# Kernel optimization log

Measured on AMD Instinct MI355X. Metric: run time of the kernel, lower is better.

## Reference

```python
import jax, jax.numpy as jnp
import numpy as np

N_LABELS = 16
LABEL_DIM = 128
BN_EPS = 1e-5


def setup_inputs() -> dict:
    key = jax.random.key(0)
    k1, k2 = jax.random.split(key, 2)
    B, T, D = 8, 512, 768
    return {
        "features": jax.random.normal(k1, (B, T, D), dtype=jnp.float32),
        "mask": jnp.ones((B, T), dtype=bool),
        "bn_gamma": jnp.ones((D,), dtype=jnp.float32),
        "bn_beta": jnp.zeros((D,), dtype=jnp.float32),
        "ff_w": jax.random.normal(k2, (LABEL_DIM * N_LABELS * 2, D), dtype=jnp.float32) * 0.02,
        "ff_b": jnp.zeros((LABEL_DIM * N_LABELS * 2,), dtype=jnp.float32),
        "label_bias": jnp.zeros((N_LABELS,), dtype=jnp.float32),
    }


def reference(features, mask, bn_gamma, bn_beta, ff_w, ff_b, label_bias):
    B, T, D = features.shape
    m = mask.astype(features.dtype)[..., None]  # [B,T,1]
    denom = jnp.maximum(m.sum(), 1.0)
    # FlatBatchNorm (training mode): stats over masked tokens, zeros elsewhere
    mean = (features * m).sum(axis=(0, 1)) / denom
    var = (((features - mean) ** 2) * m).sum(axis=(0, 1)) / denom
    normed = (features - mean) * jax.lax.rsqrt(var + BN_EPS) * bn_gamma + bn_beta
    feats = normed * m  # res[mask]=flat, zeros elsewhere
    # FFN + relu -> [B,T,n_labels,label_dim,2]
    h = jax.nn.relu(jnp.einsum('btd,od->bto', feats, ff_w) + ff_b)
    h = h.reshape(B, T, N_LABELS, LABEL_DIM, 2)
    start_f = h[..., 0]  # [B,T,L,D]
    end_f = h[..., 1]
    # biaffine span scores: [B, L, T_start, T_end]
    scores = jnp.einsum('bsld,beld->blse', start_f, end_f) + label_bias[None, :, None, None]
    triu = jnp.triu(jnp.ones((T, T), dtype=bool))
    spans_mask = triu[None, None] & mask[:, None, :, None] & mask[:, None, None, :]  # [B,L,T,T] via broadcast
    spans_mask = jnp.broadcast_to(spans_mask, scores.shape)
    return scores, spans_mask
```

## Files before the change

kernel.cpp:

```cpp
#include <hip/hip_runtime.h>

#define B_    8
#define T_    512
#define D_    768
#define L_    16
#define DL_   128
#define NO_   4096
#define M_    4096
#define BN_EPS 1e-5f

typedef __attribute__((ext_vector_type(8))) short short8;
typedef __attribute__((ext_vector_type(4))) float f32x4;

__device__ inline unsigned short f2bf(float x) {
    unsigned int u = __float_as_uint(x);
    unsigned int r = (u + 0x7fffu + ((u >> 16) & 1u)) >> 16;
    return (unsigned short)r;
}

__device__ __forceinline__ void gload_lds16(const unsigned short* g, unsigned short* l) {
    __builtin_amdgcn_global_load_lds(
        (const __attribute__((address_space(1))) unsigned int*)g,
        (__attribute__((address_space(3))) unsigned int*)l, 16, 0, 0);
}

__global__ void k_stats(const float* __restrict__ f, const int* __restrict__ mask,
                        float* __restrict__ stats) {
    int tid = threadIdx.x;
    int t0  = blockIdx.x * 16;
    float s0 = 0.f, s1 = 0.f, s2 = 0.f, q0 = 0.f, q1 = 0.f, q2 = 0.f;
    for (int tt = 0; tt < 16; ++tt) {
        int t = t0 + tt;
        float m = mask[t] ? 1.f : 0.f;
        const float* row = f + (size_t)t * D_;
        float x0 = row[tid];
        float x1 = row[tid + 256];
        float x2 = row[tid + 512];
        s0 += x0 * m; q0 += x0 * x0 * m;
        s1 += x1 * m; q1 += x1 * x1 * m;
        s2 += x2 * m; q2 += x2 * x2 * m;
    }
    atomicAdd(&stats[tid      ], s0);
    atomicAdd(&stats[tid + 256], s1);
    atomicAdd(&stats[tid + 512], s2);
    atomicAdd(&stats[768 + tid      ], q0);
    atomicAdd(&stats[768 + tid + 256], q1);
    atomicAdd(&stats[768 + tid + 512], q2);
    if (tid == 0) {
        int c = 0;
        for (int tt = 0; tt < 16; ++tt) c += (mask[t0 + tt] ? 1 : 0);
        atomicAdd(&stats[1536], (float)c);
    }
}

__global__ void k_finalize(const float* __restrict__ gamma, const float* __restrict__ beta,
                           float* __restrict__ stats) {
    int d = threadIdx.x;
    float denom = fmaxf(stats[1536], 1.f);
    float mean  = stats[d] / denom;
    float var   = fmaxf(stats[768 + d] / denom - mean * mean, 0.f);
    float sc    = gamma[d] * rsqrtf(var + BN_EPS);
    stats[2048 + d] = sc;
    stats[2816 + d] = beta[d] - mean * sc;
}

__global__ void k_normcast(const float4* __restrict__ f4, const float4* __restrict__ w4,
                           const int* __restrict__ mask, const float* __restrict__ stats,
                           unsigned short* __restrict__ featp, unsigned short* __restrict__ wp) {
    int i = blockIdx.x * 256 + threadIdx.x;
    if (i < M_ * D_ / 4) {
        int d4 = i % (D_ / 4);
        int t  = i / (D_ / 4);
        float m = mask[t] ? 1.f : 0.f;
        float4 v = f4[i];
        int d = d4 * 4;
        float r0 = (v.x * stats[2048 + d + 0] + stats[2816 + d + 0]) * m;
        float r1 = (v.y * stats[2048 + d + 1] + stats[2816 + d + 1]) * m;
        float r2 = (v.z * stats[2048 + d + 2] + stats[2816 + d + 2]) * m;
        float r3 = (v.w * stats[2048 + d + 3] + stats[2816 + d + 3]) * m;
        ushort4 o;
        o.x = f2bf(r0); o.y = f2bf(r1); o.z = f2bf(r2); o.w = f2bf(r3);
        ((ushort4*)featp)[i] = o;
    } else {
        int j = i - M_ * D_ / 4;
        float4 v = w4[j];
        ushort4 o;
        o.x = f2bf(v.x); o.y = f2bf(v.y); o.z = f2bf(v.z); o.w = f2bf(v.w);
        ((ushort4*)wp)[j] = o;
    }
}

__launch_bounds__(512, 2)
__global__ void k_ffn(const unsigned short* __restrict__ A, const unsigned short* __restrict__ W,
                      const float* __restrict__ bias,
                      unsigned short* __restrict__ startp, unsigned short* __restrict__ endp) {
    __shared__ alignas(16) unsigned short LA[4][8192];
    __shared__ alignas(16) unsigned short LB[4][8192];
    int tid  = threadIdx.x;
    int bm   = blockIdx.x, bn = blockIdx.y;
    int wave = tid >> 6, lane = tid & 63;
    int wm = wave >> 2, wn = wave & 3;
    int lr = lane & 15, quad = lane >> 4;
    int srow = lane >> 3;
    int sg   = (lane & 7) ^ srow;
    const unsigned short* asrc[2];
    const unsigned short* bsrc[2];
#pragma unroll
    for (int p = 0; p < 2; ++p) {
        int c = wave * 2 + p;
        asrc[p] = A + (size_t)(bm * 128 + c * 8 + srow) * D_ + sg * 8;
        bsrc[p] = W + (size_t)(bn * 128 + c * 8 + srow) * D_ + sg * 8;
    }
    int aoff[4][2], boff[2][2];
#pragma unroll
    for (int i = 0; i < 4; ++i)
#pragma unroll
        for (int kk = 0; kk < 2; ++kk) {
            int row = wm * 64 + i * 16 + lr;
            aoff[i][kk] = row * 64 + ((kk * 4 + quad) ^ (row & 7)) * 8;
        }
#pragma unroll
    for (int j = 0; j < 2; ++j)
#pragma unroll
        for (int kk = 0; kk < 2; ++kk) {
            int row = wn * 32 + j * 16 + lr;
            boff[j][kk] = row * 64 + ((kk * 4 + quad) ^ (row & 7)) * 8;
        }
    f32x4 acc[4][2] = {};
#pragma unroll
    for (int t = 0; t < 2; ++t) {
#pragma unroll
        for (int p = 0; p < 2; ++p) {
            int c = wave * 2 + p;
            gload_lds16(asrc[p] + t * 64, &LA[t][c * 512]);
            gload_lds16(bsrc[p] + t * 64, &LB[t][c * 512]);
        }
    }
#pragma unroll
    for (int t = 0; t < 12; ++t) {
        if (t == 11) asm volatile("s_waitcnt vmcnt(0)\ns_barrier" ::: "memory");
        else         asm volatile("s_waitcnt vmcnt(4)\ns_barrier" ::: "memory");
        const unsigned short* la = LA[t & 3];
        const unsigned short* lb = LB[t & 3];
        short8 af[4][2], bf[2][2];
#pragma unroll
        for (int i = 0; i < 4; ++i)
#pragma unroll
            for (int kk = 0; kk < 2; ++kk)
                af[i][kk] = *(const short8*)&la[aoff[i][kk]];
#pragma unroll
        for (int j = 0; j < 2; ++j)
#pragma unroll
            for (int kk = 0; kk < 2; ++kk)
                bf[j][kk] = *(const short8*)&lb[boff[j][kk]];
        if (t < 10) {
            int ss = (t + 2) & 3;
            int ko = (t + 2) * 64;
#pragma unroll
            for (int p = 0; p < 2; ++p) {
                int c = wave * 2 + p;
                gload_lds16(asrc[p] + ko, &LA[ss][c * 512]);
                gload_lds16(bsrc[p] + ko, &LB[ss][c * 512]);
            }
        }
        __builtin_amdgcn_s_setprio(1);
#pragma unroll
        for (int kk = 0; kk < 2; ++kk)
#pragma unroll
            for (int i = 0; i < 4; ++i)
#pragma unroll
                for (int j = 0; j < 2; ++j)
                    acc[i][j] = __builtin_amdgcn_mfma_f32_16x16x32_bf16(af[i][kk], bf[j][kk], acc[i][j], 0, 0, 0);
        __builtin_amdgcn_s_setprio(0);
    }
#pragma unroll
    for (int i = 0; i < 4; ++i) {
#pragma unroll
        for (int j = 0; j < 2; ++j) {
            int col  = bn * 128 + wn * 32 + j * 16 + lr;
            int l    = col >> 8;
            int dd   = (col >> 1) & 127;
            int cbit = col & 1;
            unsigned short* dst = cbit ? endp : startp;
            float bv = bias[col];
#pragma unroll
            for (int r = 0; r < 4; ++r) {
                int row = bm * 128 + wm * 64 + i * 16 + quad * 4 + r;
                float v = acc[i][j][r] + bv;
                v = fmaxf(v, 0.f);
                int bb = row >> 9, tt = row & 511;
                dst[(((size_t)(bb * 16 + l) * 512 + tt) << 7) + dd] = f2bf(v);
            }
        }
    }
}

__launch_bounds__(256)
__global__ void k_biaffine(const unsigned short* __restrict__ startp,
                           const unsigned short* __restrict__ endp,
                           const int* __restrict__ mask,
                           const float* __restrict__ lbias,
                           float* __restrict__ out_scores, float* __restrict__ out_mask) {
    __shared__ alignas(16) unsigned short As[128 * 64];
    __shared__ alignas(16) unsigned short Bs[128 * 64];
    int tid = threadIdx.x;
    int bm = blockIdx.x, bn = blockIdx.y;
    int bl = blockIdx.z;
    int b  = bl >> 4;
    const unsigned short* A  = startp + (size_t)bl * 512 * 128;
    const unsigned short* Bp = endp   + (size_t)bl * 512 * 128;
    int wave = tid >> 6, lane = tid & 63;
    int wm = wave >> 1, wn = wave & 1;
    int lr = lane & 15, quad = lane >> 4;
    f32x4 acc[4][4] = {};
    int srow = lane >> 3;
    for (int half = 0; half < 2; ++half) {
#pragma unroll
        for (int p = 0; p < 4; ++p) {
            int c   = wave * 4 + p;
            int row = c * 8 + srow;
            int gl  = (lane & 7) ^ (row & 7);
            gload_lds16(A  + (size_t)(bm * 128 + row) * DL_ + half * 64 + gl * 8, &As[c * 512]);
            gload_lds16(Bp + (size_t)(bn * 128 + row) * DL_ + half * 64 + gl * 8, &Bs[c * 512]);
        }
        __syncthreads();
#pragma unroll
        for (int kk = 0; kk < 2; ++kk) {
            short8 a[4], bb[4];
#pragma unroll
            for (int i = 0; i < 4; ++i) {
                int row = wm * 64 + i * 16 + lr;
                int gp  = (kk * 4 + quad) ^ (row & 7);
                a[i] = *(const short8*)&As[row * 64 + gp * 8];
            }
#pragma unroll
            for (int j = 0; j < 4; ++j) {
                int row = wn * 64 + j * 16 + lr;
                int gp  = (kk * 4 + quad) ^ (row & 7);
                bb[j] = *(const short8*)&Bs[row * 64 + gp * 8];
            }
#pragma unroll
            for (int i = 0; i < 4; ++i)
#pragma unroll
                for (int j = 0; j < 4; ++j)
                    acc[i][j] = __builtin_amdgcn_mfma_f32_16x16x32_bf16(a[i], bb[j], acc[i][j], 0, 0, 0);
        }
        __syncthreads();
    }
    float lb = lbias[bl & 15];
    float* obase = out_scores + (size_t)bl * 512 * 512;
    float* mbase = out_mask   + (size_t)bl * 512 * 512;
    float msv[4][4];
#pragma unroll
    for (int i = 0; i < 4; ++i)
#pragma unroll
        for (int r = 0; r < 4; ++r) {
            int s = bm * 128 + wm * 64 + i * 16 + quad * 4 + r;
            msv[i][r] = mask[b * 512 + s] ? 1.f : 0.f;
        }
#pragma unroll
    for (int j = 0; j < 4; ++j) {
        int e = bn * 128 + wn * 64 + j * 16 + lr;
        float me = mask[b * 512 + e] ? 1.f : 0.f;
#pragma unroll
        for (int i = 0; i < 4; ++i) {
#pragma unroll
            for (int r = 0; r < 4; ++r) {
                int s = bm * 128 + wm * 64 + i * 16 + quad * 4 + r;
                size_t off = (size_t)s * 512 + e;
                __builtin_nontemporal_store(acc[i][j][r] + lb, &obase[off]);
                __builtin_nontemporal_store((s <= e) ? msv[i][r] * me : 0.f, &mbase[off]);
            }
        }
    }
}

extern "C" void kernel_launch(void* const* d_in, const int* in_sizes, int n_in,
                              void* d_out, int out_size, void* d_ws, size_t ws_size,
                              hipStream_t stream) {
    const float* features = (const float*)d_in[0];
    const int*   mask     = (const int*)d_in[1];
    const float* gamma    = (const float*)d_in[2];
    const float* beta     = (const float*)d_in[3];
    const float* ffw      = (const float*)d_in[4];
    const float* ffb      = (const float*)d_in[5];
    const float* lbias    = (const float*)d_in[6];

    float* out_scores = (float*)d_out;
    float* out_mask   = out_scores + (size_t)B_ * L_ * T_ * T_;

    char* ws = (char*)d_ws;
    float*          stats  = (float*)ws;
    unsigned short* feats  = (unsigned short*)(ws + 16384);
    unsigned short* wbf    = (unsigned short*)(ws + 16384 + 6291456);
    unsigned short* startp = (unsigned short*)(ws + 12599296);
    unsigned short* endp   = (unsigned short*)(ws + 29376512);

    hipMemsetAsync(ws, 0, 16384, stream);
    k_stats<<<256, 256, 0, stream>>>(features, mask, stats);
    k_finalize<<<1, 768, 0, stream>>>(gamma, beta, stats);
    k_normcast<<<6144, 256, 0, stream>>>((const float4*)features, (const float4*)ffw,
                                         mask, stats, feats, wbf);
    dim3 g1(32, 32);
    k_ffn<<<g1, 512, 0, stream>>>(feats, wbf, ffb, startp, endp);
    dim3 g2(4, 4, 128);
    k_biaffine<<<g2, 256, 0, stream>>>(startp, endp, mask, lbias, out_scores, out_mask);
}
```

Measured before the change: 379.0 us.

## Stage biaffine output through LDS for coalesced stores; remap blocks per XCD

The biaffine epilogue now writes accumulators into shared memory (reusing the A/B tile space) and then writes full contiguous rows of scores and mask with 8-byte stores. The scattered 4-byte column stores it replaces were poorly coalesced. Both GEMM kernels also switch to a 1D grid with XCD-aware block remapping, so blocks sharing operands land on the same chiplet's L2. The extra LDS round-trip and syncs add latency in exchange for better-coalesced output writes, which dominate this write-heavy kernel.

```diff
diff --git a/kernel.cpp b/kernel.cpp
--- a/kernel.cpp
+++ b/kernel.cpp
@@ -11,6 +11,7 @@
 
 typedef __attribute__((ext_vector_type(8))) short short8;
 typedef __attribute__((ext_vector_type(4))) float f32x4;
+typedef __attribute__((ext_vector_type(2))) float f32x2;
 
 __device__ inline unsigned short f2bf(float x) {
     unsigned int u = __float_as_uint(x);
@@ -96,8 +97,11 @@
                       unsigned short* __restrict__ startp, unsigned short* __restrict__ endp) {
     __shared__ alignas(16) unsigned short LA[4][8192];
     __shared__ alignas(16) unsigned short LB[4][8192];
+    int h   = blockIdx.x;
+    int xcd = h & 7, q = h >> 3;
+    int bm  = xcd * 4 + (q >> 5);
+    int bn  = q & 31;
     int tid  = threadIdx.x;
-    int bm   = blockIdx.x, bn = blockIdx.y;
     int wave = tid >> 6, lane = tid & 63;
     int wm = wave >> 2, wn = wave & 3;
     int lr = lane & 15, quad = lane >> 4;
@@ -201,12 +205,17 @@
                            const int* __restrict__ mask,
                            const float* __restrict__ lbias,
                            float* __restrict__ out_scores, float* __restrict__ out_mask) {
-    __shared__ alignas(16) unsigned short As[128 * 64];
-    __shared__ alignas(16) unsigned short Bs[128 * 64];
+    __shared__ alignas(16) float smemf[64 * 132];
+    unsigned short* As = (unsigned short*)smemf;
+    unsigned short* Bs = As + 128 * 64;
+    float* Cs = smemf;
+    int hgrid = blockIdx.x;
+    int xcd = hgrid & 7, q = hgrid >> 3;
+    int bl  = xcd * 16 + (q >> 4);
+    int inner = q & 15;
+    int bm = inner & 3, bn = inner >> 2;
+    int b  = bl >> 4;
     int tid = threadIdx.x;
-    int bm = blockIdx.x, bn = blockIdx.y;
-    int bl = blockIdx.z;
-    int b  = bl >> 4;
     const unsigned short* A  = startp + (size_t)bl * 512 * 128;
     const unsigned short* Bp = endp   + (size_t)bl * 512 * 128;
     int wave = tid >> 6, lane = tid & 63;
@@ -250,28 +259,35 @@
     float lb = lbias[bl & 15];
     float* obase = out_scores + (size_t)bl * 512 * 512;
     float* mbase = out_mask   + (size_t)bl * 512 * 512;
-    float msv[4][4];
-#pragma unroll
-    for (int i = 0; i < 4; ++i)
-#pragma unroll
-        for (int r = 0; r < 4; ++r) {
-            int s = bm * 128 + wm * 64 + i * 16 + quad * 4 + r;
-            msv[i][r] = mask[b * 512 + s] ? 1.f : 0.f;
-        }
-#pragma unroll
-    for (int j = 0; j < 4; ++j) {
-        int e = bn * 128 + wn * 64 + j * 16 + lr;
-        float me = mask[b * 512 + e] ? 1.f : 0.f;
-#pragma unroll
-        for (int i = 0; i < 4; ++i) {
-#pragma unroll
-            for (int r = 0; r < 4; ++r) {
-                int s = bm * 128 + wm * 64 + i * 16 + quad * 4 + r;
-                size_t off = (size_t)s * 512 + e;
-                __builtin_nontemporal_store(acc[i][j][r] + lb, &obase[off]);
-                __builtin_nontemporal_store((s <= e) ? msv[i][r] * me : 0.f, &mbase[off]);
-            }
-        }
+    int e0 = bn * 128 + lane * 2;
+    float me0 = mask[b * 512 + e0    ] ? 1.f : 0.f;
+    float me1 = mask[b * 512 + e0 + 1] ? 1.f : 0.f;
+    for (int hh = 0; hh < 2; ++hh) {
+        if (wm == hh) {
+#pragma unroll
+            for (int i = 0; i < 4; ++i)
+#pragma unroll
+                for (int j = 0; j < 4; ++j)
+#pragma unroll
+                    for (int r = 0; r < 4; ++r)
+                        Cs[(i * 16 + quad * 4 + r) * 132 + wn * 64 + j * 16 + lr] = acc[i][j][r];
+        }
+        __syncthreads();
+#pragma unroll
+        for (int rr = 0; rr < 16; ++rr) {
+            int rloc = wave * 16 + rr;
+            int s = bm * 128 + hh * 64 + rloc;
+            f32x2 v = *(const f32x2*)&Cs[rloc * 132 + lane * 2];
+            v.x += lb; v.y += lb;
+            float ms = mask[b * 512 + s] ? 1.f : 0.f;
+            f32x2 mk;
+            mk.x = (s <= e0    ) ? ms * me0 : 0.f;
+            mk.y = (s <= e0 + 1) ? ms * me1 : 0.f;
+            size_t off = (size_t)s * 512 + e0;
+            __builtin_nontemporal_store(v,  (f32x2*)&obase[off]);
+            __builtin_nontemporal_store(mk, (f32x2*)&mbase[off]);
+        }
+        __syncthreads();
     }
 }
 
@@ -301,8 +317,6 @@
     k_finalize<<<1, 768, 0, stream>>>(gamma, beta, stats);
     k_normcast<<<6144, 256, 0, stream>>>((const float4*)features, (const float4*)ffw,
                                          mask, stats, feats, wbf);
-    dim3 g1(32, 32);
-    k_ffn<<<g1, 512, 0, stream>>>(feats, wbf, ffb, startp, endp);
-    dim3 g2(4, 4, 128);
-    k_biaffine<<<g2, 256, 0, stream>>>(startp, endp, mask, lbias, out_scores, out_mask);
-}
+    k_ffn<<<1024, 512, 0, stream>>>(feats, wbf, ffb, startp, endp);
+    k_biaffine<<<2048, 256, 0, stream>>>(startp, endp, mask, lbias, out_scores, out_mask);
+}
```

Measured after the change: 358.5 us. 1.06x faster.
